# Kernel tuning notes

Hardware: AMD Instinct MI355X
Metric: run time of the kernel (lower is better)

Reference implementation:

```python
import jax, jax.numpy as jnp
import numpy as np

N = 50000        # nodes
E = 800000       # edges
F_IN = 128       # input_nf == output_nf
HID = 128        # hidden_nf
HEADS = 4
HD = HID // HEADS            # 32 per-head hidden
FEAT = 2 * F_IN + 1 + 1 + 1 + 9   # 268 edge feature dim


def setup_inputs() -> dict:
    key = jax.random.key(0)
    ks = jax.random.split(key, 16)
    f32 = jnp.float32
    inp = {}
    inp["h"] = jax.random.normal(ks[0], (N, F_IN), dtype=f32)
    inp["coord"] = jax.random.normal(ks[1], (N, 3), dtype=f32)
    inp["edge_index"] = jax.random.randint(ks[2], (2, E), 0, N, dtype=jnp.int64 if jax.config.read('jax_enable_x64') else jnp.int32)
    # per-head edge MLP: Linear(FEAT,HD) -> SiLU -> Linear(HD,HD), stacked over heads
    inp["eW1"] = jax.random.normal(ks[3], (HEADS, FEAT, HD), dtype=f32) / np.sqrt(FEAT)
    inp["eb1"] = jnp.zeros((HEADS, HD), dtype=f32)
    inp["eW2"] = jax.random.normal(ks[4], (HEADS, HD, HD), dtype=f32) / np.sqrt(HD)
    inp["eb2"] = jnp.zeros((HEADS, HD), dtype=f32)
    # LayerNorm over hidden_nf
    inp["ln_g"] = jnp.ones((HID,), dtype=f32)
    inp["ln_b"] = jnp.zeros((HID,), dtype=f32)
    # node_mlp: Linear(HID+F_IN, HID) -> SiLU -> Linear(HID, F_IN)
    inp["nW1"] = jax.random.normal(ks[5], (HID + F_IN, HID), dtype=f32) / np.sqrt(HID + F_IN)
    inp["nb1"] = jnp.zeros((HID,), dtype=f32)
    inp["nW2"] = jax.random.normal(ks[6], (HID, F_IN), dtype=f32) / np.sqrt(HID)
    inp["nb2"] = jnp.zeros((F_IN,), dtype=f32)
    # coord_mlp: Linear(HID, HID) -> SiLU -> Linear(HID, 1, bias=False, xavier gain=0.001)
    inp["cW1"] = jax.random.normal(ks[7], (HID, HID), dtype=f32) / np.sqrt(HID)
    inp["cb1"] = jnp.zeros((HID,), dtype=f32)
    inp["cW2"] = jax.random.normal(ks[8], (HID, 1), dtype=f32) * 0.001
    return inp


def _forward(h, coord, edge_index, eW1, eb1, eW2, eb2, ln_g, ln_b,
             nW1, nb1, nW2, nb2, cW1, cb1, cW2):
    eps, thr = 1e-8, 1e-6
    row, col = edge_index[0], edge_index[1]
    n = h.shape[0]
    ci = coord[row]            # [E,3]
    ck = coord[col]            # [E,3]
    coord_diff = ci - ck       # rel_coord, also used for coord update
    radial = jnp.sum(coord_diff * coord_diff, axis=-1, keepdims=True)   # [E,1]
    dist = jnp.sqrt(radial)                                             # ||rel_coord||
    dot = jnp.sum(ci * ck, axis=-1, keepdims=True)                      # [E,1]
    # SO3 frame per edge
    a = coord_diff / (jnp.linalg.norm(coord_diff, axis=1, keepdims=True) + eps)
    cp = jnp.cross(ci, ck)
    b = cp / (jnp.linalg.norm(cp, axis=1, keepdims=True) + eps)
    c = jnp.cross(a, b)
    mask = ((jnp.linalg.norm(a, axis=1) < thr) |
            (jnp.linalg.norm(b, axis=1) < thr) |
            (jnp.linalg.norm(c, axis=1) < thr))
    so3 = jnp.stack([a, b, c], axis=2)                                  # [E,3,3] columns a,b,c
    so3 = jnp.where(mask[:, None, None], jnp.eye(3, dtype=so3.dtype), so3)
    so3_flat = so3.reshape(-1, 9)
    # edge features -> per-head small MLPs
    feats = jnp.concatenate([h[row], h[col], radial, dist, dot, so3_flat], axis=1)  # [E,FEAT]
    x = jax.nn.silu(jnp.einsum('ef,hfd->hed', feats, eW1) + eb1[:, None, :])
    x = jnp.einsum('hed,hdk->hek', x, eW2) + eb2[:, None, :]            # [H,E,HD]
    edge_feat = jnp.transpose(x, (1, 0, 2)).reshape(x.shape[1], -1)     # [E,HID], head-major concat
    # LayerNorm
    mu = edge_feat.mean(axis=-1, keepdims=True)
    var = edge_feat.var(axis=-1, keepdims=True)
    edge_feat = (edge_feat - mu) / jnp.sqrt(var + 1e-5) * ln_g + ln_b
    # coord update
    w = jax.nn.silu(edge_feat @ cW1 + cb1) @ cW2                        # [E,1]
    trans = coord_diff * w
    coord_out = coord + jax.ops.segment_sum(trans, row, num_segments=n)
    # node update
    agg = jax.ops.segment_sum(edge_feat, row, num_segments=n)           # [N,HID]
    y = jax.nn.silu(jnp.concatenate([h, agg], axis=1) @ nW1 + nb1) @ nW2 + nb2
    h_out = h + y                                                       # residual
    return h_out, coord_out


def reference(h, coord, edge_index, eW1, eb1, eW2, eb2, ln_g, ln_b,
              nW1, nb1, nW2, nb2, cW1, cb1, cW2):
    return _forward(h, coord, edge_index, eW1, eb1, eW2, eb2, ln_g, ln_b,
                    nW1, nb1, nW2, nb2, cW1, cb1, cW2)
```

## Files before the change

### kernel.cpp

```cpp
#include <hip/hip_runtime.h>
#include <hip/hip_bf16.h>
#include <math.h>

#define NN 50000
#define EE 800000
#define FIN 128
#define HIDN 128
#define HD 32
#define FEATD 268
#define K1 288
#define KP1 296
#define TE 32
#define TN2 64

typedef __bf16 bf16x8 __attribute__((ext_vector_type(8)));
typedef float  f32x4  __attribute__((ext_vector_type(4)));

#define MFMA(a, b, c) __builtin_amdgcn_mfma_f32_16x16x32_bf16((a), (b), (c), 0, 0, 0)

__device__ __forceinline__ float silu_f(float x) {
    const float e = __builtin_amdgcn_exp2f(-1.44269504088896f * x);
    return x * __builtin_amdgcn_rcpf(1.0f + e);
}

__device__ __forceinline__ __bf16 fbf(float x) {
    union { float f; unsigned u; } v; v.f = x;
    const unsigned r = (v.u + 0x7FFFu + ((v.u >> 16) & 1u)) >> 16;
    const unsigned short s = (unsigned short)r;
    union { unsigned short s; __bf16 b; } o; o.s = s;
    return o.b;
}

__global__ void wconv_kernel(const float* __restrict__ eW1, const float* __restrict__ eW2,
                             const float* __restrict__ cW1, const float* __restrict__ nW1,
                             const float* __restrict__ nW2,
                             __bf16* __restrict__ eW1t, __bf16* __restrict__ eW2t,
                             __bf16* __restrict__ cW1t, __bf16* __restrict__ nW1t,
                             __bf16* __restrict__ nW2t)
{
    const int i = blockIdx.x * 256 + threadIdx.x;
    if (i < 4 * 32 * K1) {
        const int hh = i / (32 * K1), rs = i % (32 * K1), d = rs / K1, k = rs % K1;
        const float v = (k < FEATD) ? eW1[(size_t)hh * FEATD * HD + (size_t)k * HD + d] : 0.f;
        eW1t[i] = (__bf16)v;
    }
    if (i < 4 * HD * HD) {
        const int hh = i / (HD * HD), rs = i % (HD * HD), d = rs / HD, k = rs % HD;
        eW2t[i] = (__bf16)eW2[(size_t)hh * HD * HD + (size_t)k * HD + d];
    }
    if (i < HIDN * HIDN) {
        const int o = i / HIDN, k = i % HIDN;
        cW1t[i] = (__bf16)cW1[(size_t)k * HIDN + o];
    }
    if (i < HIDN * (2 * FIN)) {
        const int o = i / (2 * FIN), k = i % (2 * FIN);
        nW1t[i] = (__bf16)nW1[(size_t)k * HIDN + o];
    }
    if (i < FIN * HIDN) {
        const int o = i / HIDN, k = i % HIDN;
        nW2t[i] = (__bf16)nW2[(size_t)k * FIN + o];
    }
}

__global__ __launch_bounds__(256) void hconv_kernel(const float* __restrict__ h,
                                                    float* __restrict__ houtbase)
{
    const int i = blockIdx.x * 256 + threadIdx.x;
    if (i >= NN * FIN / 8) return;
    const int row = i >> 4;
    const int c8  = i & 15;
    const float4* src = (const float4*)(h + (size_t)row * FIN + c8 * 8);
    float4 a = src[0], b = src[1];
    bf16x8 v = { fbf(a.x), fbf(a.y), fbf(a.z), fbf(a.w),
                 fbf(b.x), fbf(b.y), fbf(b.z), fbf(b.w) };
    *(bf16x8*)((char*)houtbase + (size_t)row * 512 + c8 * 16) = v;
}

__global__ __launch_bounds__(256) void edge_kernel(
    const float* __restrict__ coord,
    const int* __restrict__ ei,
    const __bf16* __restrict__ eW1t, const float* __restrict__ eb1,
    const __bf16* __restrict__ eW2t, const float* __restrict__ eb2,
    const float* __restrict__ ln_g, const float* __restrict__ ln_b,
    const __bf16* __restrict__ cW1t, const float* __restrict__ cb1,
    const float* __restrict__ cW2,
    float* __restrict__ houtbase, float* __restrict__ coord_out)
{
    __shared__ __align__(16) unsigned char smemA[TE * KP1 * 2];
    __shared__ __align__(16) unsigned char smemB[4 * TE * 40 * 2];
    __shared__ float cdiff[TE][3];
    __shared__ int   rowlds[TE];
    __shared__ float wsum[TE];

    __bf16 (*featsB)[KP1] = (__bf16 (*)[KP1])smemA;
    float  (*efs)[132]    = (float  (*)[132])smemA;
    __bf16 (*efsB)[136]   = (__bf16 (*)[136])smemB;

    const int t  = threadIdx.x;
    const int e0 = blockIdx.x * TE;

    if (t < TE) wsum[t] = 0.f;

    {
        const int e = t >> 3;
        const int q = t & 7;
        const int r = ei[e0 + e];
        const int c = ei[EE + e0 + e];
        #pragma unroll
        for (int j = 0; j < 2; j++) {
            const int c16 = q + 8 * j;
            uint4 vr = *(const uint4*)((const char*)houtbase + (size_t)r * 512 + c16 * 16);
            *(uint4*)&featsB[e][c16 * 8] = vr;
            uint4 vc = *(const uint4*)((const char*)houtbase + (size_t)c * 512 + c16 * 16);
            *(uint4*)&featsB[e][FIN + c16 * 8] = vc;
        }
        if (q == 0) {
            rowlds[e] = r;
            const float cix = coord[(size_t)r*3+0], ciy = coord[(size_t)r*3+1], ciz = coord[(size_t)r*3+2];
            const float ckx = coord[(size_t)c*3+0], cky = coord[(size_t)c*3+1], ckz = coord[(size_t)c*3+2];
            const float dx = cix-ckx, dy = ciy-cky, dz = ciz-ckz;
            cdiff[e][0]=dx; cdiff[e][1]=dy; cdiff[e][2]=dz;
            const float radial = dx*dx + dy*dy + dz*dz;
            const float dist   = sqrtf(radial);
            const float dotv   = cix*ckx + ciy*cky + ciz*ckz;
            const float ia = 1.0f / (dist + 1e-8f);
            float ax = dx*ia, ay = dy*ia, az = dz*ia;
            const float cpx = ciy*ckz - ciz*cky;
            const float cpy = ciz*ckx - cix*ckz;
            const float cpz = cix*cky - ciy*ckx;
            const float cpn = sqrtf(cpx*cpx + cpy*cpy + cpz*cpz);
            const float ib = 1.0f / (cpn + 1e-8f);
            float bx = cpx*ib, by = cpy*ib, bz = cpz*ib;
            float cx = ay*bz - az*by;
            float cy = az*bx - ax*bz;
            float cz = ax*by - ay*bx;
            const float na = sqrtf(ax*ax + ay*ay + az*az);
            const float nb = sqrtf(bx*bx + by*by + bz*bz);
            const float nc = sqrtf(cx*cx + cy*cy + cz*cz);
            if (na < 1e-6f || nb < 1e-6f || nc < 1e-6f) {
                ax=1.f; bx=0.f; cx=0.f;
                ay=0.f; by=1.f; cy=0.f;
                az=0.f; bz=0.f; cz=1.f;
            }
            featsB[e][256]=fbf(radial); featsB[e][257]=fbf(dist); featsB[e][258]=fbf(dotv);
            featsB[e][259]=fbf(ax); featsB[e][260]=fbf(bx); featsB[e][261]=fbf(cx);
            featsB[e][262]=fbf(ay); featsB[e][263]=fbf(by); featsB[e][264]=fbf(cy);
            featsB[e][265]=fbf(az); featsB[e][266]=fbf(bz); featsB[e][267]=fbf(cz);
            #pragma unroll
            for (int k = FEATD; k < K1; k++) featsB[e][k] = (__bf16)0.f;
        }
    }
    __syncthreads();

    const int hh   = t >> 6;
    const int lane = t & 63;
    const int lr   = lane & 15;
    const int lg   = lane >> 4;

    __bf16* hidB = ((__bf16*)smemB) + hh * (TE * 40);

    const f32x4 z4 = { 0.f, 0.f, 0.f, 0.f };

    {
        f32x4 acc[2][2];
        #pragma unroll
        for (int mti = 0; mti < 2; mti++) { acc[mti][0] = z4; acc[mti][1] = z4; }
        const __bf16* W1 = eW1t + (size_t)hh * 32 * K1;
        #pragma unroll
        for (int ks = 0; ks < 9; ks++) {
            const int kof = ks * 32 + lg * 8;
            bf16x8 b0 = *(const bf16x8*)(W1 + (size_t)lr * K1 + kof);
            bf16x8 b1 = *(const bf16x8*)(W1 + (size_t)(16 + lr) * K1 + kof);
            #pragma unroll
            for (int mti = 0; mti < 2; mti++) {
                bf16x8 a = *(const bf16x8*)(&featsB[mti * 16 + lr][kof]);
                acc[mti][0] = MFMA(a, b0, acc[mti][0]);
                acc[mti][1] = MFMA(a, b1, acc[mti][1]);
            }
        }
        const float b1a = eb1[hh * HD + lr];
        const float b1b = eb1[hh * HD + 16 + lr];
        #pragma unroll
        for (int mti = 0; mti < 2; mti++) {
            #pragma unroll
            for (int r = 0; r < 4; r++) {
                const int erow = mti * 16 + lg * 4 + r;
                hidB[erow * 40 + lr]      = fbf(silu_f(acc[mti][0][r] + b1a));
                hidB[erow * 40 + 16 + lr] = fbf(silu_f(acc[mti][1][r] + b1b));
            }
        }
    }
    __syncthreads();

    {
        f32x4 acc2[2][2];
        #pragma unroll
        for (int mti = 0; mti < 2; mti++) { acc2[mti][0] = z4; acc2[mti][1] = z4; }
        const __bf16* W2 = eW2t + (size_t)hh * HD * HD;
        const int kof2 = lg * 8;
        bf16x8 b20 = *(const bf16x8*)(W2 + (size_t)lr * HD + kof2);
        bf16x8 b21 = *(const bf16x8*)(W2 + (size_t)(16 + lr) * HD + kof2);
        #pragma unroll
        for (int mti = 0; mti < 2; mti++) {
            bf16x8 a = *(const bf16x8*)(hidB + (mti * 16 + lr) * 40 + kof2);
            acc2[mti][0] = MFMA(a, b20, acc2[mti][0]);
            acc2[mti][1] = MFMA(a, b21, acc2[mti][1]);
        }
        const float b2a = eb2[hh * HD + lr];
        const float b2b = eb2[hh * HD + 16 + lr];
        #pragma unroll
        for (int mti = 0; mti < 2; mti++) {
            #pragma unroll
            for (int r = 0; r < 4; r++) {
                const int erow = mti * 16 + lg * 4 + r;
                efs[erow][hh * HD + lr]      = acc2[mti][0][r] + b2a;
                efs[erow][hh * HD + 16 + lr] = acc2[mti][1][r] + b2b;
            }
        }
    }
    __syncthreads();

    {
        const int el = t >> 3;
        const int q8 = t & 7;
        const float4* src = (const float4*)&efs[el][q8 * 16];
        float4 a0 = src[0], a1 = src[1], a2 = src[2], a3 = src[3];
        float s  = a0.x+a0.y+a0.z+a0.w + a1.x+a1.y+a1.z+a1.w
                 + a2.x+a2.y+a2.z+a2.w + a3.x+a3.y+a3.z+a3.w;
        float s2 = a0.x*a0.x+a0.y*a0.y+a0.z*a0.z+a0.w*a0.w
                 + a1.x*a1.x+a1.y*a1.y+a1.z*a1.z+a1.w*a1.w
                 + a2.x*a2.x+a2.y*a2.y+a2.z*a2.z+a2.w*a2.w
                 + a3.x*a3.x+a3.y*a3.y+a3.z*a3.z+a3.w*a3.w;
        s  += __shfl_xor(s, 1);  s  += __shfl_xor(s, 2);  s  += __shfl_xor(s, 4);
        s2 += __shfl_xor(s2, 1); s2 += __shfl_xor(s2, 2); s2 += __shfl_xor(s2, 4);
        const float mu   = s * (1.f / 128.f);
        const float var  = s2 * (1.f / 128.f) - mu * mu;
        const float rstd = rsqrtf(var + 1e-5f);
        const float4* gp = (const float4*)&ln_g[q8 * 16];
        const float4* bp = (const float4*)&ln_b[q8 * 16];
        float4 g0 = gp[0], g1 = gp[1], g2 = gp[2], g3 = gp[3];
        float4 b0 = bp[0], b1 = bp[1], b2 = bp[2], b3 = bp[3];
        bf16x8 v0 = { fbf((a0.x-mu)*rstd*g0.x + b0.x), fbf((a0.y-mu)*rstd*g0.y + b0.y),
                      fbf((a0.z-mu)*rstd*g0.z + b0.z), fbf((a0.w-mu)*rstd*g0.w + b0.w),
                      fbf((a1.x-mu)*rstd*g1.x + b1.x), fbf((a1.y-mu)*rstd*g1.y + b1.y),
                      fbf((a1.z-mu)*rstd*g1.z + b1.z), fbf((a1.w-mu)*rstd*g1.w + b1.w) };
        bf16x8 v1 = { fbf((a2.x-mu)*rstd*g2.x + b2.x), fbf((a2.y-mu)*rstd*g2.y + b2.y),
                      fbf((a2.z-mu)*rstd*g2.z + b2.z), fbf((a2.w-mu)*rstd*g2.w + b2.w),
                      fbf((a3.x-mu)*rstd*g3.x + b3.x), fbf((a3.y-mu)*rstd*g3.y + b3.y),
                      fbf((a3.z-mu)*rstd*g3.z + b3.z), fbf((a3.w-mu)*rstd*g3.w + b3.w) };
        *(bf16x8*)&efsB[el][q8 * 16]     = v0;
        *(bf16x8*)&efsB[el][q8 * 16 + 8] = v1;
    }
    __syncthreads();

    {
        f32x4 acc3[2][2];
        #pragma unroll
        for (int mti = 0; mti < 2; mti++) { acc3[mti][0] = z4; acc3[mti][1] = z4; }
        const __bf16* W3 = cW1t + (size_t)hh * 32 * HIDN;
        #pragma unroll
        for (int ks = 0; ks < 4; ks++) {
            const int kof = ks * 32 + lg * 8;
            bf16x8 b30 = *(const bf16x8*)(W3 + (size_t)lr * HIDN + kof);
            bf16x8 b31 = *(const bf16x8*)(W3 + (size_t)(16 + lr) * HIDN + kof);
            #pragma unroll
            for (int mti = 0; mti < 2; mti++) {
                bf16x8 a = *(const bf16x8*)(&efsB[mti * 16 + lr][kof]);
                acc3[mti][0] = MFMA(a, b30, acc3[mti][0]);
                acc3[mti][1] = MFMA(a, b31, acc3[mti][1]);
            }
        }
        const int c0 = hh * 32 + lr, c1 = c0 + 16;
        const float cbA = cb1[c0], cbB = cb1[c1];
        const float cwA = cW2[c0], cwB = cW2[c1];
        float pe[8];
        #pragma unroll
        for (int mti = 0; mti < 2; mti++)
            #pragma unroll
            for (int r = 0; r < 4; r++)
                pe[mti * 4 + r] = silu_f(acc3[mti][0][r] + cbA) * cwA
                                + silu_f(acc3[mti][1][r] + cbB) * cwB;
        #pragma unroll
        for (int d = 1; d < 16; d <<= 1)
            #pragma unroll
            for (int i = 0; i < 8; i++) pe[i] += __shfl_xor(pe[i], d);
        if (lr == 0) {
            #pragma unroll
            for (int mti = 0; mti < 2; mti++)
                #pragma unroll
                for (int r = 0; r < 4; r++)
                    atomicAdd(&wsum[mti * 16 + lg * 4 + r], pe[mti * 4 + r]);
        }
    }
    __syncthreads();

    if (t < TE) {
        const float we = wsum[t];
        const int r = rowlds[t];
        atomicAdd(&coord_out[(size_t)r*3+0], cdiff[t][0] * we);
        atomicAdd(&coord_out[(size_t)r*3+1], cdiff[t][1] * we);
        atomicAdd(&coord_out[(size_t)r*3+2], cdiff[t][2] * we);
    }

    {
        const int p  = t & 63;
        const int gq = t >> 6;
        #pragma unroll
        for (int e2 = 0; e2 < 8; e2++) {
            const int ee = gq * 8 + e2;
            __hip_bfloat162 pk = *(__hip_bfloat162*)&efsB[ee][2 * p];
            __hip_bfloat162* addr = (__hip_bfloat162*)
                ((char*)houtbase + (size_t)rowlds[ee] * 512 + 256 + p * 4);
            unsafeAtomicAdd(addr, pk);
        }
    }
}

__global__ __launch_bounds__(512) void node_kernel(
    const float* __restrict__ h,
    const __bf16* __restrict__ nW1t, const float* __restrict__ nb1,
    const __bf16* __restrict__ nW2t, const float* __restrict__ nb2,
    float* __restrict__ h_out)
{
    __shared__ __align__(16) __bf16 featsN[TN2][264];
    __shared__ __align__(16) __bf16 hidN[TN2][136];

    const int t  = threadIdx.x;
    const int n0 = blockIdx.x * TN2;

    {
        const int n = t >> 3;
        const int q = t & 7;
        const int nid = n0 + n;
        const bool ok = nid < NN;
        const uint4* rowp = (const uint4*)((const char*)h_out + (size_t)nid * 512);
        #pragma unroll
        for (int j = 0; j < 4; j++) {
            const int w4 = q * 4 + j;
            uint4 u = ok ? rowp[w4] : make_uint4(0u, 0u, 0u, 0u);
            *(uint4*)&featsN[n][w4 * 8] = u;
        }
    }
    __syncthreads();

    const int wv2  = t >> 6;
    const int hh2  = wv2 >> 1;
    const int mh   = wv2 & 1;
    const int lane = t & 63;
    const int lr   = lane & 15;
    const int lg   = lane >> 4;

    const f32x4 z4 = { 0.f, 0.f, 0.f, 0.f };

    {
        f32x4 acc[2][2];
        #pragma unroll
        for (int mti = 0; mti < 2; mti++) { acc[mti][0] = z4; acc[mti][1] = z4; }
        const __bf16* W1 = nW1t + (size_t)hh2 * 32 * 256;
        #pragma unroll
        for (int ks = 0; ks < 8; ks++) {
            const int kof = ks * 32 + lg * 8;
            bf16x8 b0 = *(const bf16x8*)(W1 + (size_t)lr * 256 + kof);
            bf16x8 b1 = *(const bf16x8*)(W1 + (size_t)(16 + lr) * 256 + kof);
            #pragma unroll
            for (int mti = 0; mti < 2; mti++) {
                bf16x8 a = *(const bf16x8*)(&featsN[(mh * 2 + mti) * 16 + lr][kof]);
                acc[mti][0] = MFMA(a, b0, acc[mti][0]);
                acc[mti][1] = MFMA(a, b1, acc[mti][1]);
            }
        }
        const float b1a = nb1[hh2 * 32 + lr];
        const float b1b = nb1[hh2 * 32 + 16 + lr];
        #pragma unroll
        for (int mti = 0; mti < 2; mti++) {
            #pragma unroll
            for (int r = 0; r < 4; r++) {
                const int erow = (mh * 2 + mti) * 16 + lg * 4 + r;
                hidN[erow][hh2 * 32 + lr]      = fbf(silu_f(acc[mti][0][r] + b1a));
                hidN[erow][hh2 * 32 + 16 + lr] = fbf(silu_f(acc[mti][1][r] + b1b));
            }
        }
    }
    __syncthreads();

    {
        f32x4 acc2[2][2];
        #pragma unroll
        for (int mti = 0; mti < 2; mti++) { acc2[mti][0] = z4; acc2[mti][1] = z4; }
        const __bf16* W2 = nW2t + (size_t)hh2 * 32 * 128;
        #pragma unroll
        for (int ks = 0; ks < 4; ks++) {
            const int kof = ks * 32 + lg * 8;
            bf16x8 b0 = *(const bf16x8*)(W2 + (size_t)lr * 128 + kof);
            bf16x8 b1 = *(const bf16x8*)(W2 + (size_t)(16 + lr) * 128 + kof);
            #pragma unroll
            for (int mti = 0; mti < 2; mti++) {
                bf16x8 a = *(const bf16x8*)(&hidN[(mh * 2 + mti) * 16 + lr][kof]);
                acc2[mti][0] = MFMA(a, b0, acc2[mti][0]);
                acc2[mti][1] = MFMA(a, b1, acc2[mti][1]);
            }
        }
        const float b2a = nb2[hh2 * 32 + lr];
        const float b2b = nb2[hh2 * 32 + 16 + lr];
        const int c0 = hh2 * 32 + lr, c1 = c0 + 16;
        #pragma unroll
        for (int mti = 0; mti < 2; mti++) {
            #pragma unroll
            for (int r = 0; r < 4; r++) {
                const int erow = (mh * 2 + mti) * 16 + lg * 4 + r;
                const int nid  = n0 + erow;
                if (nid < NN) {
                    h_out[(size_t)nid * FIN + c0] = h[(size_t)nid * FIN + c0] + acc2[mti][0][r] + b2a;
                    h_out[(size_t)nid * FIN + c1] = h[(size_t)nid * FIN + c1] + acc2[mti][1][r] + b2b;
                }
            }
        }
    }
}

extern "C" void kernel_launch(void* const* d_in, const int* in_sizes, int n_in,
                              void* d_out, int out_size, void* d_ws, size_t ws_size,
                              hipStream_t stream)
{
    (void)in_sizes; (void)n_in; (void)out_size; (void)ws_size;
    const float* h     = (const float*)d_in[0];
    const float* coord = (const float*)d_in[1];
    const int*   ei    = (const int*)d_in[2];
    const float* eW1   = (const float*)d_in[3];
    const float* eb1   = (const float*)d_in[4];
    const float* eW2   = (const float*)d_in[5];
    const float* eb2   = (const float*)d_in[6];
    const float* ln_g  = (const float*)d_in[7];
    const float* ln_b  = (const float*)d_in[8];
    const float* nW1   = (const float*)d_in[9];
    const float* nb1   = (const float*)d_in[10];
    const float* nW2   = (const float*)d_in[11];
    const float* nb2   = (const float*)d_in[12];
    const float* cW1   = (const float*)d_in[13];
    const float* cb1   = (const float*)d_in[14];
    const float* cW2   = (const float*)d_in[15];

    float* h_out     = (float*)d_out;
    float* coord_out = h_out + (size_t)NN * FIN;

    __bf16* eW1t = (__bf16*)d_ws;
    __bf16* eW2t = eW1t + 4 * 32 * K1;
    __bf16* cW1t = eW2t + 4 * HD * HD;
    __bf16* nW1t = cW1t + HIDN * HIDN;
    __bf16* nW2t = nW1t + HIDN * (2 * FIN);

    hipMemsetAsync(h_out, 0, (size_t)NN * FIN * sizeof(float), stream);
    hipMemcpyAsync(coord_out, coord, (size_t)NN * 3 * sizeof(float),
                   hipMemcpyDeviceToDevice, stream);
    wconv_kernel<<<(4 * 32 * K1 + 255) / 256, 256, 0, stream>>>(
        eW1, eW2, cW1, nW1, nW2, eW1t, eW2t, cW1t, nW1t, nW2t);
    hconv_kernel<<<(NN * FIN / 8 + 255) / 256, 256, 0, stream>>>(h, h_out);

    edge_kernel<<<EE / TE, 256, 0, stream>>>(coord, ei, eW1t, eb1, eW2t, eb2,
                                             ln_g, ln_b, cW1t, cb1, cW2,
                                             h_out, coord_out);
    node_kernel<<<(NN + TN2 - 1) / TN2, 512, 0, stream>>>(h, nW1t, nb1, nW2t, nb2, h_out);
}
```

Before: 422.4 us.

## Process two edge tiles per block with register prefetch of second tile's gathers

Each edge block now handles 64 edges as two 32-edge tiles. The second tile's node-feature and coordinate gathers are issued into registers before the first tile's GEMMs, so gather latency overlaps with MFMA work. LayerNorm statistics are now reduced in registers via shuffles plus shared-memory atomics, which removes the fp32 edge-feature staging buffer and one barrier stage. The cost is more registers per thread, half as many blocks, and a longer serial chain of barriers inside each block.

```diff
diff --git a/kernel.cpp b/kernel.cpp
--- a/kernel.cpp
+++ b/kernel.cpp
@@ -26,8 +26,7 @@
 __device__ __forceinline__ __bf16 fbf(float x) {
     union { float f; unsigned u; } v; v.f = x;
     const unsigned r = (v.u + 0x7FFFu + ((v.u >> 16) & 1u)) >> 16;
-    const unsigned short s = (unsigned short)r;
-    union { unsigned short s; __bf16 b; } o; o.s = s;
+    union { unsigned short s; __bf16 b; } o; o.s = (unsigned short)r;
     return o.b;
 }
 
@@ -76,6 +75,183 @@
     *(bf16x8*)((char*)houtbase + (size_t)row * 512 + c8 * 16) = v;
 }
 
+__device__ __forceinline__ void geom_write(__bf16 (*featsB)[KP1], float (*cdiffp)[3],
+                                           int e, float cix, float ciy, float ciz,
+                                           float ckx, float cky, float ckz)
+{
+    const float dx = cix-ckx, dy = ciy-cky, dz = ciz-ckz;
+    cdiffp[e][0]=dx; cdiffp[e][1]=dy; cdiffp[e][2]=dz;
+    const float radial = dx*dx + dy*dy + dz*dz;
+    const float dist   = sqrtf(radial);
+    const float dotv   = cix*ckx + ciy*cky + ciz*ckz;
+    const float ia = 1.0f / (dist + 1e-8f);
+    float ax = dx*ia, ay = dy*ia, az = dz*ia;
+    const float cpx = ciy*ckz - ciz*cky;
+    const float cpy = ciz*ckx - cix*ckz;
+    const float cpz = cix*cky - ciy*ckx;
+    const float cpn = sqrtf(cpx*cpx + cpy*cpy + cpz*cpz);
+    const float ib = 1.0f / (cpn + 1e-8f);
+    float bx = cpx*ib, by = cpy*ib, bz = cpz*ib;
+    float cx = ay*bz - az*by;
+    float cy = az*bx - ax*bz;
+    float cz = ax*by - ay*bx;
+    const float na = sqrtf(ax*ax + ay*ay + az*az);
+    const float nb = sqrtf(bx*bx + by*by + bz*bz);
+    const float nc = sqrtf(cx*cx + cy*cy + cz*cz);
+    if (na < 1e-6f || nb < 1e-6f || nc < 1e-6f) {
+        ax=1.f; bx=0.f; cx=0.f;
+        ay=0.f; by=1.f; cy=0.f;
+        az=0.f; bz=0.f; cz=1.f;
+    }
+    featsB[e][256]=fbf(radial); featsB[e][257]=fbf(dist); featsB[e][258]=fbf(dotv);
+    featsB[e][259]=fbf(ax); featsB[e][260]=fbf(bx); featsB[e][261]=fbf(cx);
+    featsB[e][262]=fbf(ay); featsB[e][263]=fbf(by); featsB[e][264]=fbf(cy);
+    featsB[e][265]=fbf(az); featsB[e][266]=fbf(bz); featsB[e][267]=fbf(cz);
+    #pragma unroll
+    for (int k = FEATD; k < K1; k++) featsB[e][k] = (__bf16)0.f;
+}
+
+__device__ __forceinline__ void gemm12(const __bf16 (*featsB)[KP1], __bf16* hidB,
+                                       const __bf16* __restrict__ eW1t, const float* __restrict__ eb1,
+                                       const __bf16* __restrict__ eW2t, const float* __restrict__ eb2,
+                                       int hh, int lr, int lg, float val[2][2][4],
+                                       float (*lnSp)[2])
+{
+    const f32x4 z4 = { 0.f, 0.f, 0.f, 0.f };
+    {
+        f32x4 acc[2][2];
+        #pragma unroll
+        for (int mti = 0; mti < 2; mti++) { acc[mti][0] = z4; acc[mti][1] = z4; }
+        const __bf16* W1 = eW1t + (size_t)hh * 32 * K1;
+        #pragma unroll
+        for (int ks = 0; ks < 9; ks++) {
+            const int kof = ks * 32 + lg * 8;
+            bf16x8 b0 = *(const bf16x8*)(W1 + (size_t)lr * K1 + kof);
+            bf16x8 b1 = *(const bf16x8*)(W1 + (size_t)(16 + lr) * K1 + kof);
+            #pragma unroll
+            for (int mti = 0; mti < 2; mti++) {
+                bf16x8 a = *(const bf16x8*)(&featsB[mti * 16 + lr][kof]);
+                acc[mti][0] = MFMA(a, b0, acc[mti][0]);
+                acc[mti][1] = MFMA(a, b1, acc[mti][1]);
+            }
+        }
+        const float b1a = eb1[hh * HD + lr];
+        const float b1b = eb1[hh * HD + 16 + lr];
+        #pragma unroll
+        for (int mti = 0; mti < 2; mti++) {
+            #pragma unroll
+            for (int r = 0; r < 4; r++) {
+                const int erow = mti * 16 + lg * 4 + r;
+                hidB[erow * 40 + lr]      = fbf(silu_f(acc[mti][0][r] + b1a));
+                hidB[erow * 40 + 16 + lr] = fbf(silu_f(acc[mti][1][r] + b1b));
+            }
+        }
+    }
+    {
+        f32x4 acc2[2][2];
+        #pragma unroll
+        for (int mti = 0; mti < 2; mti++) { acc2[mti][0] = z4; acc2[mti][1] = z4; }
+        const __bf16* W2 = eW2t + (size_t)hh * HD * HD;
+        const int kof2 = lg * 8;
+        bf16x8 b20 = *(const bf16x8*)(W2 + (size_t)lr * HD + kof2);
+        bf16x8 b21 = *(const bf16x8*)(W2 + (size_t)(16 + lr) * HD + kof2);
+        #pragma unroll
+        for (int mti = 0; mti < 2; mti++) {
+            bf16x8 a = *(const bf16x8*)(hidB + (mti * 16 + lr) * 40 + kof2);
+            acc2[mti][0] = MFMA(a, b20, acc2[mti][0]);
+            acc2[mti][1] = MFMA(a, b21, acc2[mti][1]);
+        }
+        const float b2a = eb2[hh * HD + lr];
+        const float b2b = eb2[hh * HD + 16 + lr];
+        #pragma unroll
+        for (int mti = 0; mti < 2; mti++) {
+            #pragma unroll
+            for (int r = 0; r < 4; r++) {
+                val[mti][0][r] = acc2[mti][0][r] + b2a;
+                val[mti][1][r] = acc2[mti][1][r] + b2b;
+                float s  = val[mti][0][r] + val[mti][1][r];
+                float s2 = val[mti][0][r]*val[mti][0][r] + val[mti][1][r]*val[mti][1][r];
+                s  += __shfl_xor(s, 1);  s2 += __shfl_xor(s2, 1);
+                s  += __shfl_xor(s, 2);  s2 += __shfl_xor(s2, 2);
+                s  += __shfl_xor(s, 4);  s2 += __shfl_xor(s2, 4);
+                s  += __shfl_xor(s, 8);  s2 += __shfl_xor(s2, 8);
+                if (lr == 0) {
+                    const int R = mti * 16 + lg * 4 + r;
+                    atomicAdd(&lnSp[R][0], s);
+                    atomicAdd(&lnSp[R][1], s2);
+                }
+            }
+        }
+    }
+}
+
+__device__ __forceinline__ void ln_norm(const float val[2][2][4], const float (*lnSp)[2],
+                                        __bf16 (*efsB)[136],
+                                        const float* __restrict__ ln_g, const float* __restrict__ ln_b,
+                                        int hh, int lr, int lg)
+{
+    const int c0 = hh * 32 + lr, c1 = c0 + 16;
+    const float g0 = ln_g[c0], bl0 = ln_b[c0];
+    const float g1 = ln_g[c1], bl1 = ln_b[c1];
+    #pragma unroll
+    for (int mti = 0; mti < 2; mti++) {
+        #pragma unroll
+        for (int r = 0; r < 4; r++) {
+            const int R = mti * 16 + lg * 4 + r;
+            const float mu   = lnSp[R][0] * (1.f / 128.f);
+            const float var  = lnSp[R][1] * (1.f / 128.f) - mu * mu;
+            const float rstd = rsqrtf(var + 1e-5f);
+            efsB[R][c0] = fbf((val[mti][0][r] - mu) * rstd * g0 + bl0);
+            efsB[R][c1] = fbf((val[mti][1][r] - mu) * rstd * g1 + bl1);
+        }
+    }
+}
+
+__device__ __forceinline__ void gemm3_w(const __bf16 (*efsB)[136],
+                                        const __bf16* __restrict__ cW1t,
+                                        const float* __restrict__ cb1, const float* __restrict__ cW2,
+                                        int hh, int lr, int lg, float* wsump)
+{
+    const f32x4 z4 = { 0.f, 0.f, 0.f, 0.f };
+    f32x4 acc3[2][2];
+    #pragma unroll
+    for (int mti = 0; mti < 2; mti++) { acc3[mti][0] = z4; acc3[mti][1] = z4; }
+    const __bf16* W3 = cW1t + (size_t)hh * 32 * HIDN;
+    #pragma unroll
+    for (int ks = 0; ks < 4; ks++) {
+        const int kof = ks * 32 + lg * 8;
+        bf16x8 b30 = *(const bf16x8*)(W3 + (size_t)lr * HIDN + kof);
+        bf16x8 b31 = *(const bf16x8*)(W3 + (size_t)(16 + lr) * HIDN + kof);
+        #pragma unroll
+        for (int mti = 0; mti < 2; mti++) {
+            bf16x8 a = *(const bf16x8*)(&efsB[mti * 16 + lr][kof]);
+            acc3[mti][0] = MFMA(a, b30, acc3[mti][0]);
+            acc3[mti][1] = MFMA(a, b31, acc3[mti][1]);
+        }
+    }
+    const int c0 = hh * 32 + lr, c1 = c0 + 16;
+    const float cbA = cb1[c0], cbB = cb1[c1];
+    const float cwA = cW2[c0], cwB = cW2[c1];
+    float pe[8];
+    #pragma unroll
+    for (int mti = 0; mti < 2; mti++)
+        #pragma unroll
+        for (int r = 0; r < 4; r++)
+            pe[mti * 4 + r] = silu_f(acc3[mti][0][r] + cbA) * cwA
+                            + silu_f(acc3[mti][1][r] + cbB) * cwB;
+    #pragma unroll
+    for (int d = 1; d < 16; d <<= 1)
+        #pragma unroll
+        for (int i = 0; i < 8; i++) pe[i] += __shfl_xor(pe[i], d);
+    if (lr == 0) {
+        #pragma unroll
+        for (int mti = 0; mti < 2; mti++)
+            #pragma unroll
+            for (int r = 0; r < 4; r++)
+                atomicAdd(&wsump[mti * 16 + lg * 4 + r], pe[mti * 4 + r]);
+    }
+}
+
 __global__ __launch_bounds__(256) void edge_kernel(
     const float* __restrict__ coord,
     const int* __restrict__ ei,
@@ -86,222 +262,89 @@
     const float* __restrict__ cW2,
     float* __restrict__ houtbase, float* __restrict__ coord_out)
 {
-    __shared__ __align__(16) unsigned char smemA[TE * KP1 * 2];
+    __shared__ __align__(16) __bf16 featsB[TE][KP1];
     __shared__ __align__(16) unsigned char smemB[4 * TE * 40 * 2];
-    __shared__ float cdiff[TE][3];
-    __shared__ int   rowlds[TE];
-    __shared__ float wsum[TE];
-
-    __bf16 (*featsB)[KP1] = (__bf16 (*)[KP1])smemA;
-    float  (*efs)[132]    = (float  (*)[132])smemA;
-    __bf16 (*efsB)[136]   = (__bf16 (*)[136])smemB;
-
-    const int t  = threadIdx.x;
-    const int e0 = blockIdx.x * TE;
-
-    if (t < TE) wsum[t] = 0.f;
-
-    {
-        const int e = t >> 3;
-        const int q = t & 7;
-        const int r = ei[e0 + e];
-        const int c = ei[EE + e0 + e];
-        #pragma unroll
-        for (int j = 0; j < 2; j++) {
-            const int c16 = q + 8 * j;
-            uint4 vr = *(const uint4*)((const char*)houtbase + (size_t)r * 512 + c16 * 16);
-            *(uint4*)&featsB[e][c16 * 8] = vr;
-            uint4 vc = *(const uint4*)((const char*)houtbase + (size_t)c * 512 + c16 * 16);
-            *(uint4*)&featsB[e][FIN + c16 * 8] = vc;
-        }
-        if (q == 0) {
-            rowlds[e] = r;
-            const float cix = coord[(size_t)r*3+0], ciy = coord[(size_t)r*3+1], ciz = coord[(size_t)r*3+2];
-            const float ckx = coord[(size_t)c*3+0], cky = coord[(size_t)c*3+1], ckz = coord[(size_t)c*3+2];
-            const float dx = cix-ckx, dy = ciy-cky, dz = ciz-ckz;
-            cdiff[e][0]=dx; cdiff[e][1]=dy; cdiff[e][2]=dz;
-            const float radial = dx*dx + dy*dy + dz*dz;
-            const float dist   = sqrtf(radial);
-            const float dotv   = cix*ckx + ciy*cky + ciz*ckz;
-            const float ia = 1.0f / (dist + 1e-8f);
-            float ax = dx*ia, ay = dy*ia, az = dz*ia;
-            const float cpx = ciy*ckz - ciz*cky;
-            const float cpy = ciz*ckx - cix*ckz;
-            const float cpz = cix*cky - ciy*ckx;
-            const float cpn = sqrtf(cpx*cpx + cpy*cpy + cpz*cpz);
-            const float ib = 1.0f / (cpn + 1e-8f);
-            float bx = cpx*ib, by = cpy*ib, bz = cpz*ib;
-            float cx = ay*bz - az*by;
-            float cy = az*bx - ax*bz;
-            float cz = ax*by - ay*bx;
-            const float na = sqrtf(ax*ax + ay*ay + az*az);
-            const float nb = sqrtf(bx*bx + by*by + bz*bz);
-            const float nc = sqrtf(cx*cx + cy*cy + cz*cz);
-            if (na < 1e-6f || nb < 1e-6f || nc < 1e-6f) {
-                ax=1.f; bx=0.f; cx=0.f;
-                ay=0.f; by=1.f; cy=0.f;
-                az=0.f; bz=0.f; cz=1.f;
-            }
-            featsB[e][256]=fbf(radial); featsB[e][257]=fbf(dist); featsB[e][258]=fbf(dotv);
-            featsB[e][259]=fbf(ax); featsB[e][260]=fbf(bx); featsB[e][261]=fbf(cx);
-            featsB[e][262]=fbf(ay); featsB[e][263]=fbf(by); featsB[e][264]=fbf(cy);
-            featsB[e][265]=fbf(az); featsB[e][266]=fbf(bz); featsB[e][267]=fbf(cz);
-            #pragma unroll
-            for (int k = FEATD; k < K1; k++) featsB[e][k] = (__bf16)0.f;
-        }
-    }
-    __syncthreads();
-
+    __shared__ float cdiff[2][TE][3];
+    __shared__ int   rowlds[2][TE];
+    __shared__ float wsum[2][TE];
+    __shared__ float lnS[2][TE][2];
+
+    __bf16 (*efsB)[136] = (__bf16 (*)[136])smemB;
+
+    const int t    = threadIdx.x;
+    const int e0   = blockIdx.x * 64;
+    const int e    = t >> 3;
+    const int q    = t & 7;
     const int hh   = t >> 6;
     const int lane = t & 63;
     const int lr   = lane & 15;
     const int lg   = lane >> 4;
-
     __bf16* hidB = ((__bf16*)smemB) + hh * (TE * 40);
 
-    const f32x4 z4 = { 0.f, 0.f, 0.f, 0.f };
-
-    {
-        f32x4 acc[2][2];
-        #pragma unroll
-        for (int mti = 0; mti < 2; mti++) { acc[mti][0] = z4; acc[mti][1] = z4; }
-        const __bf16* W1 = eW1t + (size_t)hh * 32 * K1;
-        #pragma unroll
-        for (int ks = 0; ks < 9; ks++) {
-            const int kof = ks * 32 + lg * 8;
-            bf16x8 b0 = *(const bf16x8*)(W1 + (size_t)lr * K1 + kof);
-            bf16x8 b1 = *(const bf16x8*)(W1 + (size_t)(16 + lr) * K1 + kof);
-            #pragma unroll
-            for (int mti = 0; mti < 2; mti++) {
-                bf16x8 a = *(const bf16x8*)(&featsB[mti * 16 + lr][kof]);
-                acc[mti][0] = MFMA(a, b0, acc[mti][0]);
-                acc[mti][1] = MFMA(a, b1, acc[mti][1]);
-            }
-        }
-        const float b1a = eb1[hh * HD + lr];
-        const float b1b = eb1[hh * HD + 16 + lr];
-        #pragma unroll
-        for (int mti = 0; mti < 2; mti++) {
-            #pragma unroll
-            for (int r = 0; r < 4; r++) {
-                const int erow = mti * 16 + lg * 4 + r;
-                hidB[erow * 40 + lr]      = fbf(silu_f(acc[mti][0][r] + b1a));
-                hidB[erow * 40 + 16 + lr] = fbf(silu_f(acc[mti][1][r] + b1b));
-            }
-        }
-    }
-    __syncthreads();
-
-    {
-        f32x4 acc2[2][2];
-        #pragma unroll
-        for (int mti = 0; mti < 2; mti++) { acc2[mti][0] = z4; acc2[mti][1] = z4; }
-        const __bf16* W2 = eW2t + (size_t)hh * HD * HD;
-        const int kof2 = lg * 8;
-        bf16x8 b20 = *(const bf16x8*)(W2 + (size_t)lr * HD + kof2);
-        bf16x8 b21 = *(const bf16x8*)(W2 + (size_t)(16 + lr) * HD + kof2);
-        #pragma unroll
-        for (int mti = 0; mti < 2; mti++) {
-            bf16x8 a = *(const bf16x8*)(hidB + (mti * 16 + lr) * 40 + kof2);
-            acc2[mti][0] = MFMA(a, b20, acc2[mti][0]);
-            acc2[mti][1] = MFMA(a, b21, acc2[mti][1]);
-        }
-        const float b2a = eb2[hh * HD + lr];
-        const float b2b = eb2[hh * HD + 16 + lr];
-        #pragma unroll
-        for (int mti = 0; mti < 2; mti++) {
-            #pragma unroll
-            for (int r = 0; r < 4; r++) {
-                const int erow = mti * 16 + lg * 4 + r;
-                efs[erow][hh * HD + lr]      = acc2[mti][0][r] + b2a;
-                efs[erow][hh * HD + 16 + lr] = acc2[mti][1][r] + b2b;
-            }
-        }
-    }
-    __syncthreads();
-
-    {
-        const int el = t >> 3;
-        const int q8 = t & 7;
-        const float4* src = (const float4*)&efs[el][q8 * 16];
-        float4 a0 = src[0], a1 = src[1], a2 = src[2], a3 = src[3];
-        float s  = a0.x+a0.y+a0.z+a0.w + a1.x+a1.y+a1.z+a1.w
-                 + a2.x+a2.y+a2.z+a2.w + a3.x+a3.y+a3.z+a3.w;
-        float s2 = a0.x*a0.x+a0.y*a0.y+a0.z*a0.z+a0.w*a0.w
-                 + a1.x*a1.x+a1.y*a1.y+a1.z*a1.z+a1.w*a1.w
-                 + a2.x*a2.x+a2.y*a2.y+a2.z*a2.z+a2.w*a2.w
-                 + a3.x*a3.x+a3.y*a3.y+a3.z*a3.z+a3.w*a3.w;
-        s  += __shfl_xor(s, 1);  s  += __shfl_xor(s, 2);  s  += __shfl_xor(s, 4);
-        s2 += __shfl_xor(s2, 1); s2 += __shfl_xor(s2, 2); s2 += __shfl_xor(s2, 4);
-        const float mu   = s * (1.f / 128.f);
-        const float var  = s2 * (1.f / 128.f) - mu * mu;
-        const float rstd = rsqrtf(var + 1e-5f);
-        const float4* gp = (const float4*)&ln_g[q8 * 16];
-        const float4* bp = (const float4*)&ln_b[q8 * 16];
-        float4 g0 = gp[0], g1 = gp[1], g2 = gp[2], g3 = gp[3];
-        float4 b0 = bp[0], b1 = bp[1], b2 = bp[2], b3 = bp[3];
-        bf16x8 v0 = { fbf((a0.x-mu)*rstd*g0.x + b0.x), fbf((a0.y-mu)*rstd*g0.y + b0.y),
-                      fbf((a0.z-mu)*rstd*g0.z + b0.z), fbf((a0.w-mu)*rstd*g0.w + b0.w),
-                      fbf((a1.x-mu)*rstd*g1.x + b1.x), fbf((a1.y-mu)*rstd*g1.y + b1.y),
-                      fbf((a1.z-mu)*rstd*g1.z + b1.z), fbf((a1.w-mu)*rstd*g1.w + b1.w) };
-        bf16x8 v1 = { fbf((a2.x-mu)*rstd*g2.x + b2.x), fbf((a2.y-mu)*rstd*g2.y + b2.y),
-                      fbf((a2.z-mu)*rstd*g2.z + b2.z), fbf((a2.w-mu)*rstd*g2.w + b2.w),
-                      fbf((a3.x-mu)*rstd*g3.x + b3.x), fbf((a3.y-mu)*rstd*g3.y + b3.y),
-                      fbf((a3.z-mu)*rstd*g3.z + b3.z), fbf((a3.w-mu)*rstd*g3.w + b3.w) };
-        *(bf16x8*)&efsB[el][q8 * 16]     = v0;
-        *(bf16x8*)&efsB[el][q8 * 16 + 8] = v1;
-    }
-    __syncthreads();
-
-    {
-        f32x4 acc3[2][2];
-        #pragma unroll
-        for (int mti = 0; mti < 2; mti++) { acc3[mti][0] = z4; acc3[mti][1] = z4; }
-        const __bf16* W3 = cW1t + (size_t)hh * 32 * HIDN;
-        #pragma unroll
-        for (int ks = 0; ks < 4; ks++) {
-            const int kof = ks * 32 + lg * 8;
-            bf16x8 b30 = *(const bf16x8*)(W3 + (size_t)lr * HIDN + kof);
-            bf16x8 b31 = *(const bf16x8*)(W3 + (size_t)(16 + lr) * HIDN + kof);
-            #pragma unroll
-            for (int mti = 0; mti < 2; mti++) {
-                bf16x8 a = *(const bf16x8*)(&efsB[mti * 16 + lr][kof]);
-                acc3[mti][0] = MFMA(a, b30, acc3[mti][0]);
-                acc3[mti][1] = MFMA(a, b31, acc3[mti][1]);
-            }
-        }
-        const int c0 = hh * 32 + lr, c1 = c0 + 16;
-        const float cbA = cb1[c0], cbB = cb1[c1];
-        const float cwA = cW2[c0], cwB = cW2[c1];
-        float pe[8];
-        #pragma unroll
-        for (int mti = 0; mti < 2; mti++)
-            #pragma unroll
-            for (int r = 0; r < 4; r++)
-                pe[mti * 4 + r] = silu_f(acc3[mti][0][r] + cbA) * cwA
-                                + silu_f(acc3[mti][1][r] + cbB) * cwB;
-        #pragma unroll
-        for (int d = 1; d < 16; d <<= 1)
-            #pragma unroll
-            for (int i = 0; i < 8; i++) pe[i] += __shfl_xor(pe[i], d);
-        if (lr == 0) {
-            #pragma unroll
-            for (int mti = 0; mti < 2; mti++)
-                #pragma unroll
-                for (int r = 0; r < 4; r++)
-                    atomicAdd(&wsum[mti * 16 + lg * 4 + r], pe[mti * 4 + r]);
-        }
-    }
-    __syncthreads();
-
+    const int r0 = ei[e0 + e],      c0v = ei[EE + e0 + e];
+    const int r1 = ei[e0 + 32 + e], c1v = ei[EE + e0 + 32 + e];
+
+    if (t < TE) { wsum[0][t] = 0.f; lnS[0][t][0] = 0.f; lnS[0][t][1] = 0.f; }
+    {
+        #pragma unroll
+        for (int j = 0; j < 2; j++) {
+            const int c16 = q + 8 * j;
+            uint4 vr = *(const uint4*)((const char*)houtbase + (size_t)r0 * 512 + c16 * 16);
+            *(uint4*)&featsB[e][c16 * 8] = vr;
+            uint4 vc = *(const uint4*)((const char*)houtbase + (size_t)c0v * 512 + c16 * 16);
+            *(uint4*)&featsB[e][FIN + c16 * 8] = vc;
+        }
+        if (q == 0) {
+            rowlds[0][e] = r0;
+            geom_write(featsB, cdiff[0], e,
+                       coord[(size_t)r0*3+0], coord[(size_t)r0*3+1], coord[(size_t)r0*3+2],
+                       coord[(size_t)c0v*3+0], coord[(size_t)c0v*3+1], coord[(size_t)c0v*3+2]);
+        }
+    }
+    __syncthreads();
+
+    uint4 vr1[2], vc1[2];
+    #pragma unroll
+    for (int j = 0; j < 2; j++) {
+        const int c16 = q + 8 * j;
+        vr1[j] = *(const uint4*)((const char*)houtbase + (size_t)r1 * 512 + c16 * 16);
+        vc1[j] = *(const uint4*)((const char*)houtbase + (size_t)c1v * 512 + c16 * 16);
+    }
+    float cf1[6] = {0.f,0.f,0.f,0.f,0.f,0.f};
+    if (q == 0) {
+        cf1[0] = coord[(size_t)r1*3+0]; cf1[1] = coord[(size_t)r1*3+1]; cf1[2] = coord[(size_t)r1*3+2];
+        cf1[3] = coord[(size_t)c1v*3+0]; cf1[4] = coord[(size_t)c1v*3+1]; cf1[5] = coord[(size_t)c1v*3+2];
+    }
+
+    float val0[2][2][4];
+    gemm12(featsB, hidB, eW1t, eb1, eW2t, eb2, hh, lr, lg, val0, lnS[0]);
+    __syncthreads();
+
+    if (t < TE) { wsum[1][t] = 0.f; lnS[1][t][0] = 0.f; lnS[1][t][1] = 0.f; }
+    {
+        #pragma unroll
+        for (int j = 0; j < 2; j++) {
+            const int c16 = q + 8 * j;
+            *(uint4*)&featsB[e][c16 * 8]       = vr1[j];
+            *(uint4*)&featsB[e][FIN + c16 * 8] = vc1[j];
+        }
+        if (q == 0) {
+            rowlds[1][e] = r1;
+            geom_write(featsB, cdiff[1], e, cf1[0], cf1[1], cf1[2], cf1[3], cf1[4], cf1[5]);
+        }
+    }
+    ln_norm(val0, lnS[0], efsB, ln_g, ln_b, hh, lr, lg);
+    __syncthreads();
+
+    gemm3_w(efsB, cW1t, cb1, cW2, hh, lr, lg, wsum[0]);
+    __syncthreads();
     if (t < TE) {
-        const float we = wsum[t];
-        const int r = rowlds[t];
-        atomicAdd(&coord_out[(size_t)r*3+0], cdiff[t][0] * we);
-        atomicAdd(&coord_out[(size_t)r*3+1], cdiff[t][1] * we);
-        atomicAdd(&coord_out[(size_t)r*3+2], cdiff[t][2] * we);
-    }
-
+        const float we = wsum[0][t];
+        const int r = rowlds[0][t];
+        atomicAdd(&coord_out[(size_t)r*3+0], cdiff[0][t][0] * we);
+        atomicAdd(&coord_out[(size_t)r*3+1], cdiff[0][t][1] * we);
+        atomicAdd(&coord_out[(size_t)r*3+2], cdiff[0][t][2] * we);
+    }
     {
         const int p  = t & 63;
         const int gq = t >> 6;
@@ -310,7 +353,35 @@
             const int ee = gq * 8 + e2;
             __hip_bfloat162 pk = *(__hip_bfloat162*)&efsB[ee][2 * p];
             __hip_bfloat162* addr = (__hip_bfloat162*)
-                ((char*)houtbase + (size_t)rowlds[ee] * 512 + 256 + p * 4);
+                ((char*)houtbase + (size_t)rowlds[0][ee] * 512 + 256 + p * 4);
+            unsafeAtomicAdd(addr, pk);
+        }
+    }
+    __syncthreads();
+
+    float val1[2][2][4];
+    gemm12(featsB, hidB, eW1t, eb1, eW2t, eb2, hh, lr, lg, val1, lnS[1]);
+    __syncthreads();
+    ln_norm(val1, lnS[1], efsB, ln_g, ln_b, hh, lr, lg);
+    __syncthreads();
+    gemm3_w(efsB, cW1t, cb1, cW2, hh, lr, lg, wsum[1]);
+    __syncthreads();
+    if (t < TE) {
+        const float we = wsum[1][t];
+        const int r = rowlds[1][t];
+        atomicAdd(&coord_out[(size_t)r*3+0], cdiff[1][t][0] * we);
+        atomicAdd(&coord_out[(size_t)r*3+1], cdiff[1][t][1] * we);
+        atomicAdd(&coord_out[(size_t)r*3+2], cdiff[1][t][2] * we);
+    }
+    {
+        const int p  = t & 63;
+        const int gq = t >> 6;
+        #pragma unroll
+        for (int e2 = 0; e2 < 8; e2++) {
+            const int ee = gq * 8 + e2;
+            __hip_bfloat162 pk = *(__hip_bfloat162*)&efsB[ee][2 * p];
+            __hip_bfloat162* addr = (__hip_bfloat162*)
+                ((char*)houtbase + (size_t)rowlds[1][ee] * 512 + 256 + p * 4);
             unsafeAtomicAdd(addr, pk);
         }
     }
@@ -456,7 +527,7 @@
         eW1, eW2, cW1, nW1, nW2, eW1t, eW2t, cW1t, nW1t, nW2t);
     hconv_kernel<<<(NN * FIN / 8 + 255) / 256, 256, 0, stream>>>(h, h_out);
 
-    edge_kernel<<<EE / TE, 256, 0, stream>>>(coord, ei, eW1t, eb1, eW2t, eb2,
+    edge_kernel<<<EE / 64, 256, 0, stream>>>(coord, ei, eW1t, eb1, eW2t, eb2,
                                              ln_g, ln_b, cW1t, cb1, cW2,
                                              h_out, coord_out);
     node_kernel<<<(NN + TN2 - 1) / TN2, 512, 0, stream>>>(h, nW1t, nb1, nW2t, nb2, h_out);
```

After: 458.1 us. +8.4%, slower.

## Fuse LayerNorm statistics into second edge GEMM epilogue and hoist scatter atomics

Applied to the files above, without the earlier changes.

The second edge-MLP GEMM now keeps its outputs in registers and reduces per-row sum and sum-of-squares with wave shuffles plus LDS atomics. This removes the fp32 staging buffer in shared memory, a separate LayerNorm pass, and one barrier (the barrier between the two edge GEMMs is also dropped). The bf16 atomic scatter of edge features into node rows is moved ahead of the coord-MLP GEMM so its global traffic can overlap that compute. The cost is extra shuffles and shared-memory float atomics per row, and the barrier removed between GEMM1's hidB writes and GEMM2's reads relies on each wave touching only its own head slice.

```diff
diff --git a/kernel.cpp b/kernel.cpp
--- a/kernel.cpp
+++ b/kernel.cpp
@@ -26,8 +26,7 @@
 __device__ __forceinline__ __bf16 fbf(float x) {
     union { float f; unsigned u; } v; v.f = x;
     const unsigned r = (v.u + 0x7FFFu + ((v.u >> 16) & 1u)) >> 16;
-    const unsigned short s = (unsigned short)r;
-    union { unsigned short s; __bf16 b; } o; o.s = s;
+    union { unsigned short s; __bf16 b; } o; o.s = (unsigned short)r;
     return o.b;
 }
 
@@ -86,20 +85,19 @@
     const float* __restrict__ cW2,
     float* __restrict__ houtbase, float* __restrict__ coord_out)
 {
-    __shared__ __align__(16) unsigned char smemA[TE * KP1 * 2];
+    __shared__ __align__(16) __bf16 featsB[TE][KP1];
     __shared__ __align__(16) unsigned char smemB[4 * TE * 40 * 2];
     __shared__ float cdiff[TE][3];
     __shared__ int   rowlds[TE];
     __shared__ float wsum[TE];
-
-    __bf16 (*featsB)[KP1] = (__bf16 (*)[KP1])smemA;
-    float  (*efs)[132]    = (float  (*)[132])smemA;
-    __bf16 (*efsB)[136]   = (__bf16 (*)[136])smemB;
+    __shared__ float lnS[TE][2];
+
+    __bf16 (*efsB)[136] = (__bf16 (*)[136])smemB;
 
     const int t  = threadIdx.x;
     const int e0 = blockIdx.x * TE;
 
-    if (t < TE) wsum[t] = 0.f;
+    if (t < TE) { wsum[t] = 0.f; lnS[t][0] = 0.f; lnS[t][1] = 0.f; }
 
     {
         const int e = t >> 3;
@@ -156,11 +154,11 @@
     const int lane = t & 63;
     const int lr   = lane & 15;
     const int lg   = lane >> 4;
-
     __bf16* hidB = ((__bf16*)smemB) + hh * (TE * 40);
 
     const f32x4 z4 = { 0.f, 0.f, 0.f, 0.f };
 
+    float val[2][2][4];
     {
         f32x4 acc[2][2];
         #pragma unroll
@@ -189,10 +187,6 @@
                 hidB[erow * 40 + 16 + lr] = fbf(silu_f(acc[mti][1][r] + b1b));
             }
         }
-    }
-    __syncthreads();
-
-    {
         f32x4 acc2[2][2];
         #pragma unroll
         for (int mti = 0; mti < 2; mti++) { acc2[mti][0] = z4; acc2[mti][1] = z4; }
@@ -212,46 +206,55 @@
         for (int mti = 0; mti < 2; mti++) {
             #pragma unroll
             for (int r = 0; r < 4; r++) {
-                const int erow = mti * 16 + lg * 4 + r;
-                efs[erow][hh * HD + lr]      = acc2[mti][0][r] + b2a;
-                efs[erow][hh * HD + 16 + lr] = acc2[mti][1][r] + b2b;
-            }
-        }
-    }
-    __syncthreads();
-
-    {
-        const int el = t >> 3;
-        const int q8 = t & 7;
-        const float4* src = (const float4*)&efs[el][q8 * 16];
-        float4 a0 = src[0], a1 = src[1], a2 = src[2], a3 = src[3];
-        float s  = a0.x+a0.y+a0.z+a0.w + a1.x+a1.y+a1.z+a1.w
-                 + a2.x+a2.y+a2.z+a2.w + a3.x+a3.y+a3.z+a3.w;
-        float s2 = a0.x*a0.x+a0.y*a0.y+a0.z*a0.z+a0.w*a0.w
-                 + a1.x*a1.x+a1.y*a1.y+a1.z*a1.z+a1.w*a1.w
-                 + a2.x*a2.x+a2.y*a2.y+a2.z*a2.z+a2.w*a2.w
-                 + a3.x*a3.x+a3.y*a3.y+a3.z*a3.z+a3.w*a3.w;
-        s  += __shfl_xor(s, 1);  s  += __shfl_xor(s, 2);  s  += __shfl_xor(s, 4);
-        s2 += __shfl_xor(s2, 1); s2 += __shfl_xor(s2, 2); s2 += __shfl_xor(s2, 4);
-        const float mu   = s * (1.f / 128.f);
-        const float var  = s2 * (1.f / 128.f) - mu * mu;
-        const float rstd = rsqrtf(var + 1e-5f);
-        const float4* gp = (const float4*)&ln_g[q8 * 16];
-        const float4* bp = (const float4*)&ln_b[q8 * 16];
-        float4 g0 = gp[0], g1 = gp[1], g2 = gp[2], g3 = gp[3];
-        float4 b0 = bp[0], b1 = bp[1], b2 = bp[2], b3 = bp[3];
-        bf16x8 v0 = { fbf((a0.x-mu)*rstd*g0.x + b0.x), fbf((a0.y-mu)*rstd*g0.y + b0.y),
-                      fbf((a0.z-mu)*rstd*g0.z + b0.z), fbf((a0.w-mu)*rstd*g0.w + b0.w),
-                      fbf((a1.x-mu)*rstd*g1.x + b1.x), fbf((a1.y-mu)*rstd*g1.y + b1.y),
-                      fbf((a1.z-mu)*rstd*g1.z + b1.z), fbf((a1.w-mu)*rstd*g1.w + b1.w) };
-        bf16x8 v1 = { fbf((a2.x-mu)*rstd*g2.x + b2.x), fbf((a2.y-mu)*rstd*g2.y + b2.y),
-                      fbf((a2.z-mu)*rstd*g2.z + b2.z), fbf((a2.w-mu)*rstd*g2.w + b2.w),
-                      fbf((a3.x-mu)*rstd*g3.x + b3.x), fbf((a3.y-mu)*rstd*g3.y + b3.y),
-                      fbf((a3.z-mu)*rstd*g3.z + b3.z), fbf((a3.w-mu)*rstd*g3.w + b3.w) };
-        *(bf16x8*)&efsB[el][q8 * 16]     = v0;
-        *(bf16x8*)&efsB[el][q8 * 16 + 8] = v1;
-    }
-    __syncthreads();
+                val[mti][0][r] = acc2[mti][0][r] + b2a;
+                val[mti][1][r] = acc2[mti][1][r] + b2b;
+                float s  = val[mti][0][r] + val[mti][1][r];
+                float s2 = val[mti][0][r]*val[mti][0][r] + val[mti][1][r]*val[mti][1][r];
+                s  += __shfl_xor(s, 1);  s2 += __shfl_xor(s2, 1);
+                s  += __shfl_xor(s, 2);  s2 += __shfl_xor(s2, 2);
+                s  += __shfl_xor(s, 4);  s2 += __shfl_xor(s2, 4);
+                s  += __shfl_xor(s, 8);  s2 += __shfl_xor(s2, 8);
+                if (lr == 0) {
+                    const int R = mti * 16 + lg * 4 + r;
+                    atomicAdd(&lnS[R][0], s);
+                    atomicAdd(&lnS[R][1], s2);
+                }
+            }
+        }
+    }
+    __syncthreads();
+
+    {
+        const int c0 = hh * 32 + lr, c1 = c0 + 16;
+        const float g0 = ln_g[c0], bl0 = ln_b[c0];
+        const float g1 = ln_g[c1], bl1 = ln_b[c1];
+        #pragma unroll
+        for (int mti = 0; mti < 2; mti++) {
+            #pragma unroll
+            for (int r = 0; r < 4; r++) {
+                const int R = mti * 16 + lg * 4 + r;
+                const float mu   = lnS[R][0] * (1.f / 128.f);
+                const float var  = lnS[R][1] * (1.f / 128.f) - mu * mu;
+                const float rstd = rsqrtf(var + 1e-5f);
+                efsB[R][c0] = fbf((val[mti][0][r] - mu) * rstd * g0 + bl0);
+                efsB[R][c1] = fbf((val[mti][1][r] - mu) * rstd * g1 + bl1);
+            }
+        }
+    }
+    __syncthreads();
+
+    {
+        const int p  = t & 63;
+        const int gq = t >> 6;
+        #pragma unroll
+        for (int e2 = 0; e2 < 8; e2++) {
+            const int ee = gq * 8 + e2;
+            __hip_bfloat162 pk = *(__hip_bfloat162*)&efsB[ee][2 * p];
+            __hip_bfloat162* addr = (__hip_bfloat162*)
+                ((char*)houtbase + (size_t)rowlds[ee] * 512 + 256 + p * 4);
+            unsafeAtomicAdd(addr, pk);
+        }
+    }
 
     {
         f32x4 acc3[2][2];
@@ -300,19 +303,6 @@
         atomicAdd(&coord_out[(size_t)r*3+0], cdiff[t][0] * we);
         atomicAdd(&coord_out[(size_t)r*3+1], cdiff[t][1] * we);
         atomicAdd(&coord_out[(size_t)r*3+2], cdiff[t][2] * we);
-    }
-
-    {
-        const int p  = t & 63;
-        const int gq = t >> 6;
-        #pragma unroll
-        for (int e2 = 0; e2 < 8; e2++) {
-            const int ee = gq * 8 + e2;
-            __hip_bfloat162 pk = *(__hip_bfloat162*)&efsB[ee][2 * p];
-            __hip_bfloat162* addr = (__hip_bfloat162*)
-                ((char*)houtbase + (size_t)rowlds[ee] * 512 + 256 + p * 4);
-            unsafeAtomicAdd(addr, pk);
-        }
     }
 }
 
```

New measurement: 412.7 us (median of 3 runs). 1.02x faster.
